# Kernel tuning notes

Measured on AMD Instinct MI355X. Metric: run time of the kernel, lower is better.

Reference implementation:

```python
import jax, jax.numpy as jnp
import numpy as np

B, S, I, H = 1, 4096, 4096, 4096  # batch, seq_len(=input_size), input_size, hidden_size


def setup_inputs() -> dict:
    key = jax.random.key(0)
    ks = jax.random.split(key, 6)
    sc = 1.0 / np.sqrt(H).astype(np.float32)
    x = jax.random.normal(ks[0], (B, I), jnp.float32)
    hidden = jax.random.normal(ks[1], (B, H), jnp.float32)
    # PyTorch GRUCell params, gate order [r, z, n]
    w_ih = jax.random.uniform(ks[2], (3 * H, I), jnp.float32, -sc, sc)
    w_hh = jax.random.uniform(ks[3], (3 * H, H), jnp.float32, -sc, sc)
    b_ih = jax.random.uniform(ks[4], (3 * H,), jnp.float32, -sc, sc)
    b_hh = jax.random.uniform(ks[5], (3 * H,), jnp.float32, -sc, sc)
    return {"x": x, "hidden": hidden, "w_ih": w_ih, "w_hh": w_hh, "b_ih": b_ih, "b_hh": b_hh}


def gru_cell(x, h, w_ih, w_hh, b_ih, b_hh):
    gi = x @ w_ih.T + b_ih  # [B, 3H]
    gh = h @ w_hh.T + b_hh  # [B, 3H]
    i_r, i_z, i_n = jnp.split(gi, 3, axis=-1)
    h_r, h_z, h_n = jnp.split(gh, 3, axis=-1)
    r = jax.nn.sigmoid(i_r + h_r)
    z = jax.nn.sigmoid(i_z + h_z)
    n = jnp.tanh(i_n + r * h_n)
    return (1.0 - z) * h + z * n  # [B, H]


def reference(x, hidden, w_ih, w_hh, b_ih, b_hh):
    seq_len = x.shape[1]
    b = gru_cell(x, hidden, w_ih, w_hh, b_ih, b_hh)  # [B, H]
    a = jax.nn.relu(b)  # relu(b[:, t]) for all t at once

    # out_0 = relu(b[:,0]) + roll(hidden, 1, -1); [B] + [B,H] broadcasts (B==1)
    out0 = a[:, 0] + jnp.roll(hidden, 1, axis=-1)  # [B, H]

    def step(prev, a_t):  # prev: [B, H], a_t: [B]
        out = a_t + jnp.roll(prev, 1, axis=-1)
        return out, out

    _, rest = jax.lax.scan(step, out0, a[:, 1:seq_len].T)  # rest: [S-1, B, H]
    outputs = jnp.concatenate([out0[:, None], jnp.moveaxis(rest, 0, 1)], axis=1)  # [B, S, H]
    new_hidden = outputs[:, -1, :]
    # torch .squeeze(2) is a no-op since H != 1
    return outputs, new_hidden
```

## Files before the change

kernel.cpp:

```cpp
#include <hip/hip_runtime.h>


#define H4 4096
#define R3 12288

__global__ __launch_bounds__(256) void gemv_kernel(
    const float* __restrict__ x,
    const float* __restrict__ hidden,
    const float* __restrict__ w_ih,
    const float* __restrict__ w_hh,
    const float* __restrict__ b_ih,
    const float* __restrict__ b_hh,
    float* __restrict__ g) {
  __shared__ float4 vs[1024];

  const int block = blockIdx.x;
  const bool isX = (block < 768);
  const float* vec  = isX ? x    : hidden;
  const float* wmat = isX ? w_ih : w_hh;
  const float* bias = isX ? b_ih : b_hh;
  const int rowb = (isX ? block : block - 768) * 16;
  const int gbase = isX ? 0 : R3;

  const float4* vv = reinterpret_cast<const float4*>(vec);
#pragma unroll
  for (int i = 0; i < 4; ++i) {
    const int idx = i * 256 + threadIdx.x;
    vs[idx] = vv[idx];
  }
  __syncthreads();

  const int wid = threadIdx.x >> 6;
  const int lane = threadIdx.x & 63;
  const int row0 = rowb + wid * 4;
  const float4* w0 = reinterpret_cast<const float4*>(wmat + (size_t)row0 * H4);

  float4 acc0 = {0.f, 0.f, 0.f, 0.f};
  float4 acc1 = {0.f, 0.f, 0.f, 0.f};
  float4 acc2 = {0.f, 0.f, 0.f, 0.f};
  float4 acc3 = {0.f, 0.f, 0.f, 0.f};

#pragma unroll
  for (int it = 0; it < 16; ++it) {
    const int idx = it * 64 + lane;
    const float4 v4 = vs[idx];
    const float4 wq0 = w0[idx];
    const float4 wq1 = w0[1024 + idx];
    const float4 wq2 = w0[2048 + idx];
    const float4 wq3 = w0[3072 + idx];
    acc0.x = fmaf(wq0.x, v4.x, acc0.x); acc0.y = fmaf(wq0.y, v4.y, acc0.y);
    acc0.z = fmaf(wq0.z, v4.z, acc0.z); acc0.w = fmaf(wq0.w, v4.w, acc0.w);
    acc1.x = fmaf(wq1.x, v4.x, acc1.x); acc1.y = fmaf(wq1.y, v4.y, acc1.y);
    acc1.z = fmaf(wq1.z, v4.z, acc1.z); acc1.w = fmaf(wq1.w, v4.w, acc1.w);
    acc2.x = fmaf(wq2.x, v4.x, acc2.x); acc2.y = fmaf(wq2.y, v4.y, acc2.y);
    acc2.z = fmaf(wq2.z, v4.z, acc2.z); acc2.w = fmaf(wq2.w, v4.w, acc2.w);
    acc3.x = fmaf(wq3.x, v4.x, acc3.x); acc3.y = fmaf(wq3.y, v4.y, acc3.y);
    acc3.z = fmaf(wq3.z, v4.z, acc3.z); acc3.w = fmaf(wq3.w, v4.w, acc3.w);
  }

  float s0 = (acc0.x + acc0.y) + (acc0.z + acc0.w);
  float s1 = (acc1.x + acc1.y) + (acc1.z + acc1.w);
  float s2 = (acc2.x + acc2.y) + (acc2.z + acc2.w);
  float s3 = (acc3.x + acc3.y) + (acc3.z + acc3.w);
#pragma unroll
  for (int d = 32; d > 0; d >>= 1) {
    s0 += __shfl_down(s0, d, 64);
    s1 += __shfl_down(s1, d, 64);
    s2 += __shfl_down(s2, d, 64);
    s3 += __shfl_down(s3, d, 64);
  }
  if (lane == 0) {
    g[gbase + row0 + 0] = s0 + bias[row0 + 0];
    g[gbase + row0 + 1] = s1 + bias[row0 + 1];
    g[gbase + row0 + 2] = s2 + bias[row0 + 2];
    g[gbase + row0 + 3] = s3 + bias[row0 + 3];
  }
}

__global__ __launch_bounds__(1024) void combine_scan_kernel(
    const float* __restrict__ hidden,
    const float* __restrict__ g,
    float* __restrict__ prefix,
    float* __restrict__ out_newh) {
  const int tid = threadIdx.x;
  const int s0 = tid * 4;

  const float4 gir = reinterpret_cast<const float4*>(g)[tid];
  const float4 giz = reinterpret_cast<const float4*>(g + H4)[tid];
  const float4 gin = reinterpret_cast<const float4*>(g + 2 * H4)[tid];
  const float4 ghr = reinterpret_cast<const float4*>(g + R3)[tid];
  const float4 ghz = reinterpret_cast<const float4*>(g + R3 + H4)[tid];
  const float4 ghn = reinterpret_cast<const float4*>(g + R3 + 2 * H4)[tid];
  const float4 h4v = reinterpret_cast<const float4*>(hidden)[tid];

  const float ir[4] = {gir.x, gir.y, gir.z, gir.w};
  const float iz[4] = {giz.x, giz.y, giz.z, giz.w};
  const float in_[4] = {gin.x, gin.y, gin.z, gin.w};
  const float hr[4] = {ghr.x, ghr.y, ghr.z, ghr.w};
  const float hz[4] = {ghz.x, ghz.y, ghz.z, ghz.w};
  const float hn[4] = {ghn.x, ghn.y, ghn.z, ghn.w};
  const float hh[4] = {h4v.x, h4v.y, h4v.z, h4v.w};

  float a[4];
#pragma unroll
  for (int k = 0; k < 4; ++k) {
    const float r = 1.f / (1.f + __expf(-(ir[k] + hr[k])));
    const float z = 1.f / (1.f + __expf(-(iz[k] + hz[k])));
    const float n = tanhf(in_[k] + r * hn[k]);
    const float b = (1.f - z) * hh[k] + z * n;
    a[k] = fmaxf(b, 0.f);
  }
  const float c0 = a[0], c1 = c0 + a[1], c2 = c1 + a[2], c3 = c2 + a[3];
  const float tsum = c3;

  const int lane = tid & 63, wid = tid >> 6;
  float v = tsum;
#pragma unroll
  for (int d = 1; d < 64; d <<= 1) {
    float o = __shfl_up(v, d, 64);
    if (lane >= d) v += o;
  }
  __shared__ float wsum[16];
  if (lane == 63) wsum[wid] = v;
  __syncthreads();
  if (tid < 16) {
    float w = wsum[tid];
#pragma unroll
    for (int d = 1; d < 16; d <<= 1) {
      float o = __shfl_up(w, d, 64);
      if (tid >= d) w += o;
    }
    wsum[tid] = w;
  }
  __syncthreads();

  const float excl = (wid ? wsum[wid - 1] : 0.f) + (v - tsum);
  float4 pr;
  pr.x = excl + c0; pr.y = excl + c1; pr.z = excl + c2; pr.w = excl + c3;
  reinterpret_cast<float4*>(prefix)[tid] = pr;

  const float total = wsum[15];
  float4 nh;
  nh.x = total + hh[0]; nh.y = total + hh[1];
  nh.z = total + hh[2]; nh.w = total + hh[3];
  reinterpret_cast<float4*>(out_newh)[tid] = nh;
}

__global__ __launch_bounds__(256) void outputs_kernel(
    const float* __restrict__ prefix,
    const float* __restrict__ hidden,
    float* __restrict__ out) {
  const int b = blockIdx.x;
  const int t = b >> 1;
  const int j0 = (b & 1) * 2048 + threadIdx.x * 8;
  const float p = prefix[t];
  const int base = (j0 - t - 1) & 4095;

  float4 o0, o1;
  o0.x = p + hidden[base];
  o0.y = p + hidden[(base + 1) & 4095];
  o0.z = p + hidden[(base + 2) & 4095];
  o0.w = p + hidden[(base + 3) & 4095];
  o1.x = p + hidden[(base + 4) & 4095];
  o1.y = p + hidden[(base + 5) & 4095];
  o1.z = p + hidden[(base + 6) & 4095];
  o1.w = p + hidden[(base + 7) & 4095];

  float* dst = out + (size_t)t * H4 + j0;
  *reinterpret_cast<float4*>(dst)     = o0;
  *reinterpret_cast<float4*>(dst + 4) = o1;
}

extern "C" void kernel_launch(void* const* d_in, const int* in_sizes, int n_in,
                              void* d_out, int out_size, void* d_ws, size_t ws_size,
                              hipStream_t stream) {
  const float* x      = (const float*)d_in[0];
  const float* hidden = (const float*)d_in[1];
  const float* w_ih   = (const float*)d_in[2];
  const float* w_hh   = (const float*)d_in[3];
  const float* b_ih   = (const float*)d_in[4];
  const float* b_hh   = (const float*)d_in[5];
  float* out = (float*)d_out;

  float* ws     = (float*)d_ws;
  float* g      = ws;
  float* prefix = ws + 24576;

  gemv_kernel<<<1536, 256, 0, stream>>>(x, hidden, w_ih, w_hh, b_ih, b_hh, g);
  combine_scan_kernel<<<1, 1024, 0, stream>>>(hidden, g, prefix,
                                              out + (size_t)H4 * H4);
  outputs_kernel<<<8192, 256, 0, stream>>>(prefix, hidden, out);
}
```

Before: 448.8 us.

## Restructure GEMV so each thread holds vector slice in registers across 16 rows

The GEMV block no longer stages the input vector in shared memory. Each thread keeps its 16 floats of the vector in registers and accumulates 16 rows, reading the weights with a block-wide stride. The per-row partial sums are reduced with wavefront shuffles and then a small shared-memory cross-wave sum. Launch bounds now request 6 blocks per multiprocessor to raise occupancy. The cost is 16 accumulators plus 16 vector values per thread and sixteen sequential shuffle reductions.

```diff
diff --git a/kernel.cpp b/kernel.cpp
--- a/kernel.cpp
+++ b/kernel.cpp
@@ -4,7 +4,7 @@
 #define H4 4096
 #define R3 12288
 
-__global__ __launch_bounds__(256) void gemv_kernel(
+__global__ __launch_bounds__(256, 6) void gemv_kernel(
     const float* __restrict__ x,
     const float* __restrict__ hidden,
     const float* __restrict__ w_ih,
@@ -12,8 +12,6 @@
     const float* __restrict__ b_ih,
     const float* __restrict__ b_hh,
     float* __restrict__ g) {
-  __shared__ float4 vs[1024];
-
   const int block = blockIdx.x;
   const bool isX = (block < 768);
   const float* vec  = isX ? x    : hidden;
@@ -22,58 +20,46 @@
   const int rowb = (isX ? block : block - 768) * 16;
   const int gbase = isX ? 0 : R3;
 
+  const int tid = threadIdx.x;
+  const int lane = tid & 63;
+  const int wid = tid >> 6;
+
   const float4* vv = reinterpret_cast<const float4*>(vec);
+  float4 vk[4];
 #pragma unroll
-  for (int i = 0; i < 4; ++i) {
-    const int idx = i * 256 + threadIdx.x;
-    vs[idx] = vv[idx];
+  for (int k = 0; k < 4; ++k) vk[k] = vv[k * 256 + tid];
+
+  const float4* wp =
+      reinterpret_cast<const float4*>(wmat) + (size_t)rowb * 1024 + tid;
+
+  float acc[16];
+#pragma unroll
+  for (int r = 0; r < 16; ++r) acc[r] = 0.f;
+
+#pragma unroll
+  for (int r = 0; r < 16; ++r) {
+#pragma unroll
+    for (int k = 0; k < 4; ++k) {
+      const float4 wq = wp[(r * 4 + k) * 256];
+      acc[r] = fmaf(wq.x, vk[k].x, acc[r]);
+      acc[r] = fmaf(wq.y, vk[k].y, acc[r]);
+      acc[r] = fmaf(wq.z, vk[k].z, acc[r]);
+      acc[r] = fmaf(wq.w, vk[k].w, acc[r]);
+    }
+  }
+
+  __shared__ float red[64];
+#pragma unroll
+  for (int r = 0; r < 16; ++r) {
+    float s = acc[r];
+#pragma unroll
+    for (int d = 32; d > 0; d >>= 1) s += __shfl_down(s, d, 64);
+    if (lane == 0) red[wid * 16 + r] = s;
   }
   __syncthreads();
-
-  const int wid = threadIdx.x >> 6;
-  const int lane = threadIdx.x & 63;
-  const int row0 = rowb + wid * 4;
-  const float4* w0 = reinterpret_cast<const float4*>(wmat + (size_t)row0 * H4);
-
-  float4 acc0 = {0.f, 0.f, 0.f, 0.f};
-  float4 acc1 = {0.f, 0.f, 0.f, 0.f};
-  float4 acc2 = {0.f, 0.f, 0.f, 0.f};
-  float4 acc3 = {0.f, 0.f, 0.f, 0.f};
-
-#pragma unroll
-  for (int it = 0; it < 16; ++it) {
-    const int idx = it * 64 + lane;
-    const float4 v4 = vs[idx];
-    const float4 wq0 = w0[idx];
-    const float4 wq1 = w0[1024 + idx];
-    const float4 wq2 = w0[2048 + idx];
-    const float4 wq3 = w0[3072 + idx];
-    acc0.x = fmaf(wq0.x, v4.x, acc0.x); acc0.y = fmaf(wq0.y, v4.y, acc0.y);
-    acc0.z = fmaf(wq0.z, v4.z, acc0.z); acc0.w = fmaf(wq0.w, v4.w, acc0.w);
-    acc1.x = fmaf(wq1.x, v4.x, acc1.x); acc1.y = fmaf(wq1.y, v4.y, acc1.y);
-    acc1.z = fmaf(wq1.z, v4.z, acc1.z); acc1.w = fmaf(wq1.w, v4.w, acc1.w);
-    acc2.x = fmaf(wq2.x, v4.x, acc2.x); acc2.y = fmaf(wq2.y, v4.y, acc2.y);
-    acc2.z = fmaf(wq2.z, v4.z, acc2.z); acc2.w = fmaf(wq2.w, v4.w, acc2.w);
-    acc3.x = fmaf(wq3.x, v4.x, acc3.x); acc3.y = fmaf(wq3.y, v4.y, acc3.y);
-    acc3.z = fmaf(wq3.z, v4.z, acc3.z); acc3.w = fmaf(wq3.w, v4.w, acc3.w);
-  }
-
-  float s0 = (acc0.x + acc0.y) + (acc0.z + acc0.w);
-  float s1 = (acc1.x + acc1.y) + (acc1.z + acc1.w);
-  float s2 = (acc2.x + acc2.y) + (acc2.z + acc2.w);
-  float s3 = (acc3.x + acc3.y) + (acc3.z + acc3.w);
-#pragma unroll
-  for (int d = 32; d > 0; d >>= 1) {
-    s0 += __shfl_down(s0, d, 64);
-    s1 += __shfl_down(s1, d, 64);
-    s2 += __shfl_down(s2, d, 64);
-    s3 += __shfl_down(s3, d, 64);
-  }
-  if (lane == 0) {
-    g[gbase + row0 + 0] = s0 + bias[row0 + 0];
-    g[gbase + row0 + 1] = s1 + bias[row0 + 1];
-    g[gbase + row0 + 2] = s2 + bias[row0 + 2];
-    g[gbase + row0 + 3] = s3 + bias[row0 + 3];
+  if (tid < 16) {
+    const float v = (red[tid] + red[16 + tid]) + (red[32 + tid] + red[48 + tid]);
+    g[gbase + rowb + tid] = v + bias[rowb + tid];
   }
 }
 
@@ -83,7 +69,6 @@
     float* __restrict__ prefix,
     float* __restrict__ out_newh) {
   const int tid = threadIdx.x;
-  const int s0 = tid * 4;
 
   const float4 gir = reinterpret_cast<const float4*>(g)[tid];
   const float4 giz = reinterpret_cast<const float4*>(g + H4)[tid];
```

Measured after the change: 573.7 us. 1.28x slower.
